# Optimization experiments

Hardware: AMD Instinct MI355X
Metric: run time of the kernel (lower is better)

Reference implementation:

```python
import jax, jax.numpy as jnp
import numpy as np
from jax import lax

B, N, C = 16, 16384, 256
NP, NS = 128, 16        # num_proposal, nsample
R = 0.3                 # ball radius (normalize_xyz divides by R)


def setup_inputs() -> dict:
    key = jax.random.key(0)
    ks = jax.random.split(key, 11)
    f32 = jnp.float32
    return dict(
        vote_xyz=jax.random.uniform(ks[0], (B, N, 3), f32),
        vote_features=jax.random.normal(ks[1], (B, C, N), f32),
        # SA shared-MLP 1x1 conv weights (bias folded into BN), mlp=[259,128,128,128]
        W1=jax.random.normal(ks[2], (128, C + 3), f32) * 0.05,
        W2=jax.random.normal(ks[3], (128, 128), f32) * 0.05,
        W3=jax.random.normal(ks[4], (128, 128), f32) * 0.05,
        sa_bn_scale=jax.random.uniform(ks[5], (3, 128), f32, 0.5, 1.5),
        sa_bn_bias=jax.random.normal(ks[6], (3, 128), f32) * 0.1,
        # trailing mlp_module: two Conv1d(128,128,1)+BN(eval)+ReLU
        Wm=jax.random.normal(ks[7], (2, 128, 128), f32) * 0.05,
        bm=jax.random.normal(ks[8], (2, 128), f32) * 0.01,
        m_bn_scale=jax.random.uniform(ks[9], (2, 128), f32, 0.5, 1.5),
        m_bn_bias=jax.random.normal(ks[10], (2, 128), f32) * 0.1,
    )


def _fps(xyz):
    # farthest point sampling, one cloud: xyz [N,3] -> inds [NP]
    def body(carry, _):
        mind, last = carry
        d = jnp.sum((xyz - xyz[last]) ** 2, axis=-1)
        mind = jnp.minimum(mind, d)
        nxt = jnp.argmax(mind).astype(jnp.int32)
        return (mind, nxt), nxt
    init = (jnp.full((xyz.shape[0],), 1e10, xyz.dtype), jnp.int32(0))
    _, rest = lax.scan(body, init, None, length=NP - 1)
    return jnp.concatenate([jnp.zeros((1,), jnp.int32), rest])


def _ball_query(xyz, centers):
    # xyz [N,3], centers [NP,3] -> idx [NP,NS]; first NS in-ball points in
    # original order, padded with the first in-ball index (pointnet2 semantics)
    d2 = jnp.sum((centers[:, None, :] - xyz[None, :, :]) ** 2, axis=-1)  # [NP,N]
    n = xyz.shape[0]
    cand = jnp.where(d2 < R * R, jnp.arange(n, dtype=jnp.int32), jnp.int32(n))
    firstk = jnp.sort(cand, axis=-1)[:, :NS]                             # [NP,NS]
    first = firstk[:, :1]
    idx = jnp.where(firstk == n, first, firstk)
    return jnp.where(idx == n, 0, idx)


def _forward(vote_xyz, vote_features, W1, W2, W3, sa_bn_scale, sa_bn_bias,
             Wm, bm, m_bn_scale, m_bn_bias):
    fps_inds = jax.vmap(_fps)(vote_xyz)                                   # [B,NP]
    new_xyz = jnp.take_along_axis(vote_xyz, fps_inds[..., None], axis=1)  # [B,NP,3]
    idx = jax.vmap(_ball_query)(vote_xyz, new_xyz)                        # [B,NP,NS]
    grouped_xyz = jax.vmap(lambda p, i: p[i])(vote_xyz, idx)              # [B,NP,NS,3]
    grouped_xyz = (grouped_xyz - new_xyz[:, :, None, :]) / R              # normalize_xyz
    grouped_feat = jax.vmap(lambda f, i: f[:, i])(vote_features, idx)     # [B,C,NP,NS]
    g = jnp.concatenate([grouped_xyz.transpose(0, 3, 1, 2), grouped_feat], axis=1)  # [B,C+3,NP,NS]
    for W, s, b in ((W1, sa_bn_scale[0], sa_bn_bias[0]),
                    (W2, sa_bn_scale[1], sa_bn_bias[1]),
                    (W3, sa_bn_scale[2], sa_bn_bias[2])):
        g = jax.nn.relu(jnp.einsum('bcsn,oc->bosn', g, W)
                        * s[None, :, None, None] + b[None, :, None, None])
    feat = jnp.max(g, axis=-1)                                            # [B,128,NP] max pool
    for k in range(2):
        feat = jax.nn.relu((jnp.einsum('bcs,oc->bos', feat, Wm[k]) + bm[k][None, :, None])
                           * m_bn_scale[k][None, :, None] + m_bn_bias[k][None, :, None])
    return new_xyz, feat, fps_inds


def reference(vote_xyz, vote_features, W1, W2, W3, sa_bn_scale, sa_bn_bias,
              Wm, bm, m_bn_scale, m_bn_bias):
    return _forward(vote_xyz, vote_features, W1, W2, W3, sa_bn_scale, sa_bn_bias,
                    Wm, bm, m_bn_scale, m_bn_bias)
```

## Files before the change

### kernel.cpp

```cpp
#include <hip/hip_runtime.h>
#include <hip/hip_bf16.h>

#define NB  16
#define NN  16384
#define NC  256
#define NPP 128
#define NSS 16

#define FTH 1024
#define FPT 16

__global__ __launch_bounds__(256) void transpose_kernel(
    const float* __restrict__ W1, const float* __restrict__ W2,
    const float* __restrict__ W3, const float* __restrict__ Wm,
    float* __restrict__ W1T, float* __restrict__ W2T,
    float* __restrict__ W3T, float* __restrict__ WmT) {
  int i = blockIdx.x * 256 + threadIdx.x;
  if (i < 128 * 259) { int o = i / 259, c = i - o * 259; W1T[c * 128 + o] = W1[i]; }
  if (i < 128 * 128) {
    int o = i >> 7, c = i & 127;
    W2T[c * 128 + o] = W2[i];
    W3T[c * 128 + o] = W3[i];
    WmT[c * 128 + o] = Wm[i];
    WmT[16384 + c * 128 + o] = Wm[16384 + i];
  }
}

__global__ __attribute__((amdgpu_flat_work_group_size(1024, 1024)))
void fps_kernel(
    const float* __restrict__ xyz,
    float* __restrict__ centers, float* __restrict__ out_xyz,
    float* __restrict__ out_indf) {
  int b = blockIdx.x;
  const float* px = xyz + (size_t)b * (NN * 3);
  int t = threadIdx.x;
  __shared__ float2 sxy[NN];
  __shared__ unsigned long long cand[2][16];
  __shared__ float zcand[2][16];
  __shared__ float4 hist[NPP];
  float Zr[FPT], MD[FPT];
#pragma unroll
  for (int j = 0; j < FPT; ++j) {
    int n = t + j * FTH;
    float x = px[n * 3 + 0];
    float y = px[n * 3 + 1];
    float z = px[n * 3 + 2];
    asm volatile("" : "+v"(z));
    sxy[n] = make_float2(x, y);
    Zr[j] = z;
    MD[j] = 1e10f;
  }
  float cx = px[0], cy = px[1], cz = px[2];
  if (t == 0) hist[0] = make_float4(cx, cy, cz, 0.0f);
  __syncthreads();
  for (int it = 1; it < NPP; ++it) {
    float bv = -1.0f;
    float bz = 0.0f;
    int bj = 0;
#pragma unroll
    for (int j = 0; j < FPT; ++j) {
      float2 v = sxy[t + j * FTH];
      float dx = __fsub_rn(v.x, cx);
      float dy = __fsub_rn(v.y, cy);
      float dz = __fsub_rn(Zr[j], cz);
      float d  = __fadd_rn(__fadd_rn(__fmul_rn(dx, dx), __fmul_rn(dy, dy)),
                           __fmul_rn(dz, dz));
      float m = fminf(MD[j], d);
      MD[j] = m;
      if (m > bv) { bv = m; bj = j; bz = Zr[j]; }
    }
    int bi = t + (bj << 10);
    unsigned long long pk =
        (((unsigned long long)__float_as_uint(bv)) << 32) |
        (unsigned long long)(~(unsigned)bi);
#define STEP_ROR(N)                                                         \
    {                                                                       \
      unsigned lo = (unsigned)pk, hi = (unsigned)(pk >> 32);                \
      lo = (unsigned)__builtin_amdgcn_mov_dpp((int)lo, 0x120 | N, 0xF, 0xF, true); \
      hi = (unsigned)__builtin_amdgcn_mov_dpp((int)hi, 0x120 | N, 0xF, 0xF, true); \
      float oz = __int_as_float(__builtin_amdgcn_mov_dpp(                   \
          __float_as_int(bz), 0x120 | N, 0xF, 0xF, true));                  \
      unsigned long long o = ((unsigned long long)hi << 32) | lo;           \
      if (o > pk) { pk = o; bz = oz; }                                      \
    }
    STEP_ROR(1) STEP_ROR(2) STEP_ROR(4) STEP_ROR(8)
    {
      unsigned lo = (unsigned)pk, hi = (unsigned)(pk >> 32);
      lo = (unsigned)__builtin_amdgcn_ds_swizzle((int)lo, 0x401F);
      hi = (unsigned)__builtin_amdgcn_ds_swizzle((int)hi, 0x401F);
      float oz = __int_as_float(
          __builtin_amdgcn_ds_swizzle(__float_as_int(bz), 0x401F));
      unsigned long long o = ((unsigned long long)hi << 32) | lo;
      if (o > pk) { pk = o; bz = oz; }
    }
    {
      unsigned long long o = __shfl_xor(pk, 32, 64);
      float oz = __shfl_xor(bz, 32, 64);
      if (o > pk) { pk = o; bz = oz; }
    }
    int p = it & 1;
    if ((t & 63) == 0) { cand[p][t >> 6] = pk; zcand[p][t >> 6] = bz; }
    __syncthreads();
    pk = cand[p][t & 15];
    bz = zcand[p][t & 15];
    STEP_ROR(1) STEP_ROR(2) STEP_ROR(4) STEP_ROR(8)
#undef STEP_ROR
    int win = (int)(~(unsigned)(pk & 0xFFFFFFFFull));
    win = __builtin_amdgcn_readfirstlane(win);
    float2 wv = sxy[win];
    cx = wv.x;
    cy = wv.y;
    cz = bz;
    if (t == 0) hist[it] = make_float4(cx, cy, cz, (float)win);
  }
  __syncthreads();
  if (t < NPP) {
    float4 h = hist[t];
    centers[(b * NPP + t) * 3 + 0] = h.x;
    centers[(b * NPP + t) * 3 + 1] = h.y;
    centers[(b * NPP + t) * 3 + 2] = h.z;
    out_xyz[(b * NPP + t) * 3 + 0] = h.x;
    out_xyz[(b * NPP + t) * 3 + 1] = h.y;
    out_xyz[(b * NPP + t) * 3 + 2] = h.z;
    out_indf[b * NPP + t] = h.w;
  }
}

__global__ __launch_bounds__(64) void ballq_kernel(
    const float* __restrict__ xyz, const float* __restrict__ centers,
    int* __restrict__ bidx) {
  int bs = blockIdx.x;
  int b = bs >> 7;
  int lane = threadIdx.x;
  const float* px = xyz + (size_t)b * (NN * 3);
  float cx = centers[bs * 3 + 0];
  float cy = centers[bs * 3 + 1];
  float cz = centers[bs * 3 + 2];
  __shared__ int coll[NSS];
  const float rr = 0.09f;
  int have = 0;
  for (int c0 = 0; c0 < NN; c0 += 64) {
    int n = c0 + lane;
    float dx = __fsub_rn(px[n * 3 + 0], cx);
    float dy = __fsub_rn(px[n * 3 + 1], cy);
    float dz = __fsub_rn(px[n * 3 + 2], cz);
    float d2 = __fadd_rn(__fadd_rn(__fmul_rn(dx, dx), __fmul_rn(dy, dy)),
                         __fmul_rn(dz, dz));
    bool in = d2 < rr;
    unsigned long long m = __ballot(in);
    if (in) {
      int pos = have + __popcll(m & ((1ull << lane) - 1ull));
      if (pos < NSS) coll[pos] = n;
    }
    have += __popcll(m);
    if (have >= NSS) break;
  }
  __syncthreads();
  int first = coll[0];
  if (lane < NSS) bidx[bs * NSS + lane] = (lane < have) ? coll[lane] : first;
}

__device__ __forceinline__ void layer_f(const float (*in)[20], int cin,
                                        const float* __restrict__ WT,
                                        const float* __restrict__ sc,
                                        const float* __restrict__ bi,
                                        int o2, int k0, float4& r0, float4& r1) {
  float a0[4] = {0.f, 0.f, 0.f, 0.f};
  float a1[4] = {0.f, 0.f, 0.f, 0.f};
  for (int c = 0; c < cin; ++c) {
    float2 w = *(const float2*)(WT + c * 128 + o2);
    float4 gv = *(const float4*)(&in[c][k0]);
    a0[0] = fmaf(w.x, gv.x, a0[0]);
    a0[1] = fmaf(w.x, gv.y, a0[1]);
    a0[2] = fmaf(w.x, gv.z, a0[2]);
    a0[3] = fmaf(w.x, gv.w, a0[3]);
    a1[0] = fmaf(w.y, gv.x, a1[0]);
    a1[1] = fmaf(w.y, gv.y, a1[1]);
    a1[2] = fmaf(w.y, gv.z, a1[2]);
    a1[3] = fmaf(w.y, gv.w, a1[3]);
  }
  float s0 = sc[o2], s1 = sc[o2 + 1], b0 = bi[o2], b1 = bi[o2 + 1];
  r0.x = fmaxf(fmaf(a0[0], s0, b0), 0.f);
  r0.y = fmaxf(fmaf(a0[1], s0, b0), 0.f);
  r0.z = fmaxf(fmaf(a0[2], s0, b0), 0.f);
  r0.w = fmaxf(fmaf(a0[3], s0, b0), 0.f);
  r1.x = fmaxf(fmaf(a1[0], s1, b1), 0.f);
  r1.y = fmaxf(fmaf(a1[1], s1, b1), 0.f);
  r1.z = fmaxf(fmaf(a1[2], s1, b1), 0.f);
  r1.w = fmaxf(fmaf(a1[3], s1, b1), 0.f);
}

__global__ __launch_bounds__(256) void mlp_kernel(
    const float* __restrict__ xyz, const float* __restrict__ feats,
    const float* __restrict__ centers, const int* __restrict__ bidx,
    const float* __restrict__ W1T, const float* __restrict__ W2T,
    const float* __restrict__ W3T, const float* __restrict__ sa_sc,
    const float* __restrict__ sa_bi, float* __restrict__ feat0) {
  int bs = blockIdx.x;
  int b = bs >> 7;
  int s = bs & 127;
  int tid = threadIdx.x;
  __shared__ float g[259][20];
  __shared__ float h1[128][20];
  __shared__ float h2[128][20];
  __shared__ int kidx[NSS];
  __shared__ float ctr[3];
  if (tid < NSS) kidx[tid] = bidx[bs * NSS + tid];
  if (tid < 3) ctr[tid] = centers[bs * 3 + tid];
  __syncthreads();
  const float* px = xyz + (size_t)b * (NN * 3);
  if (tid < NSS) {
    int n = kidx[tid];
    g[0][tid] = __fdiv_rn(__fsub_rn(px[n * 3 + 0], ctr[0]), 0.3f);
    g[1][tid] = __fdiv_rn(__fsub_rn(px[n * 3 + 1], ctr[1]), 0.3f);
    g[2][tid] = __fdiv_rn(__fsub_rn(px[n * 3 + 2], ctr[2]), 0.3f);
  }
  {
    const float* row = feats + ((size_t)b * NC + tid) * NN;
#pragma unroll
    for (int k = 0; k < NSS; ++k) g[3 + tid][k] = row[kidx[k]];
  }
  __syncthreads();
  int o2 = (tid & 63) * 2;
  int k0 = (tid >> 6) * 4;
  float4 r0, r1;
  layer_f(g, 259, W1T, sa_sc, sa_bi, o2, k0, r0, r1);
  *(float4*)&h1[o2][k0] = r0;
  *(float4*)&h1[o2 + 1][k0] = r1;
  __syncthreads();
  layer_f(h1, 128, W2T, sa_sc + 128, sa_bi + 128, o2, k0, r0, r1);
  *(float4*)&h2[o2][k0] = r0;
  *(float4*)&h2[o2 + 1][k0] = r1;
  __syncthreads();
  layer_f(h2, 128, W3T, sa_sc + 256, sa_bi + 256, o2, k0, r0, r1);
  float m0 = fmaxf(fmaxf(r0.x, r0.y), fmaxf(r0.z, r0.w));
  float m1 = fmaxf(fmaxf(r1.x, r1.y), fmaxf(r1.z, r1.w));
  int w = tid >> 6;
  h1[o2][w] = m0;
  h1[o2 + 1][w] = m1;
  __syncthreads();
  if (tid < 128) {
    float m = fmaxf(fmaxf(h1[tid][0], h1[tid][1]), fmaxf(h1[tid][2], h1[tid][3]));
    feat0[((size_t)b * 128 + tid) * 128 + s] = m;
  }
}

__global__ __launch_bounds__(256) void head_kernel(
    const float* __restrict__ feat0, const float* __restrict__ WmT,
    const float* __restrict__ bm, const float* __restrict__ msc,
    const float* __restrict__ mbi, float* __restrict__ out_feat) {
  int blk = blockIdx.x;
  int b = blk >> 2;
  int sbase = (blk & 3) * 32;
  int tid = threadIdx.x;
  __shared__ float fa[128][36];
  __shared__ float fb[128][36];
  {
    int sj = tid & 31, c0 = tid >> 5;
    for (int c = c0; c < 128; c += 8)
      fa[c][sj] = feat0[((size_t)b * 128 + c) * 128 + sbase + sj];
  }
  __syncthreads();
  int o2 = (tid & 63) * 2, s0 = (tid >> 6) * 8;
  float a0[8], a1[8];
#pragma unroll
  for (int j = 0; j < 8; ++j) { a0[j] = 0.f; a1[j] = 0.f; }
  for (int c = 0; c < 128; ++c) {
    float2 w = *(const float2*)&WmT[c * 128 + o2];
    float4 f0 = *(const float4*)&fa[c][s0];
    float4 f1 = *(const float4*)&fa[c][s0 + 4];
    a0[0] = fmaf(w.x, f0.x, a0[0]); a0[1] = fmaf(w.x, f0.y, a0[1]);
    a0[2] = fmaf(w.x, f0.z, a0[2]); a0[3] = fmaf(w.x, f0.w, a0[3]);
    a0[4] = fmaf(w.x, f1.x, a0[4]); a0[5] = fmaf(w.x, f1.y, a0[5]);
    a0[6] = fmaf(w.x, f1.z, a0[6]); a0[7] = fmaf(w.x, f1.w, a0[7]);
    a1[0] = fmaf(w.y, f0.x, a1[0]); a1[1] = fmaf(w.y, f0.y, a1[1]);
    a1[2] = fmaf(w.y, f0.z, a1[2]); a1[3] = fmaf(w.y, f0.w, a1[3]);
    a1[4] = fmaf(w.y, f1.x, a1[4]); a1[5] = fmaf(w.y, f1.y, a1[5]);
    a1[6] = fmaf(w.y, f1.z, a1[6]); a1[7] = fmaf(w.y, f1.w, a1[7]);
  }
  {
    float c0 = bm[o2], c1 = bm[o2 + 1];
    float t0 = msc[o2], t1 = msc[o2 + 1];
    float q0 = mbi[o2], q1 = mbi[o2 + 1];
#pragma unroll
    for (int j = 0; j < 8; ++j) {
      fb[o2][s0 + j]     = fmaxf(fmaf(a0[j] + c0, t0, q0), 0.f);
      fb[o2 + 1][s0 + j] = fmaxf(fmaf(a1[j] + c1, t1, q1), 0.f);
    }
  }
  __syncthreads();
#pragma unroll
  for (int j = 0; j < 8; ++j) { a0[j] = 0.f; a1[j] = 0.f; }
  for (int c = 0; c < 128; ++c) {
    float2 w = *(const float2*)&WmT[16384 + c * 128 + o2];
    float4 f0 = *(const float4*)&fb[c][s0];
    float4 f1 = *(const float4*)&fb[c][s0 + 4];
    a0[0] = fmaf(w.x, f0.x, a0[0]); a0[1] = fmaf(w.x, f0.y, a0[1]);
    a0[2] = fmaf(w.x, f0.z, a0[2]); a0[3] = fmaf(w.x, f0.w, a0[3]);
    a0[4] = fmaf(w.x, f1.x, a0[4]); a0[5] = fmaf(w.x, f1.y, a0[5]);
    a0[6] = fmaf(w.x, f1.z, a0[6]); a0[7] = fmaf(w.x, f1.w, a0[7]);
    a1[0] = fmaf(w.y, f0.x, a1[0]); a1[1] = fmaf(w.y, f0.y, a1[1]);
    a1[2] = fmaf(w.y, f0.z, a1[2]); a1[3] = fmaf(w.y, f0.w, a1[3]);
    a1[4] = fmaf(w.y, f1.x, a1[4]); a1[5] = fmaf(w.y, f1.y, a1[5]);
    a1[6] = fmaf(w.y, f1.z, a1[6]); a1[7] = fmaf(w.y, f1.w, a1[7]);
  }
  {
    float c0 = bm[128 + o2], c1 = bm[128 + o2 + 1];
    float t0 = msc[128 + o2], t1 = msc[128 + o2 + 1];
    float q0 = mbi[128 + o2], q1 = mbi[128 + o2 + 1];
    float4 v0a, v0b, v1a, v1b;
    v0a.x = fmaxf(fmaf(a0[0] + c0, t0, q0), 0.f);
    v0a.y = fmaxf(fmaf(a0[1] + c0, t0, q0), 0.f);
    v0a.z = fmaxf(fmaf(a0[2] + c0, t0, q0), 0.f);
    v0a.w = fmaxf(fmaf(a0[3] + c0, t0, q0), 0.f);
    v0b.x = fmaxf(fmaf(a0[4] + c0, t0, q0), 0.f);
    v0b.y = fmaxf(fmaf(a0[5] + c0, t0, q0), 0.f);
    v0b.z = fmaxf(fmaf(a0[6] + c0, t0, q0), 0.f);
    v0b.w = fmaxf(fmaf(a0[7] + c0, t0, q0), 0.f);
    v1a.x = fmaxf(fmaf(a1[0] + c1, t1, q1), 0.f);
    v1a.y = fmaxf(fmaf(a1[1] + c1, t1, q1), 0.f);
    v1a.z = fmaxf(fmaf(a1[2] + c1, t1, q1), 0.f);
    v1a.w = fmaxf(fmaf(a1[3] + c1, t1, q1), 0.f);
    v1b.x = fmaxf(fmaf(a1[4] + c1, t1, q1), 0.f);
    v1b.y = fmaxf(fmaf(a1[5] + c1, t1, q1), 0.f);
    v1b.z = fmaxf(fmaf(a1[6] + c1, t1, q1), 0.f);
    v1b.w = fmaxf(fmaf(a1[7] + c1, t1, q1), 0.f);
    float* p0 = &out_feat[((size_t)b * 128 + o2) * 128 + sbase + s0];
    float* p1 = &out_feat[((size_t)b * 128 + o2 + 1) * 128 + sbase + s0];
    *(float4*)p0 = v0a;
    *(float4*)(p0 + 4) = v0b;
    *(float4*)p1 = v1a;
    *(float4*)(p1 + 4) = v1b;
  }
}

extern "C" void kernel_launch(void* const* d_in, const int* in_sizes, int n_in,
                              void* d_out, int out_size, void* d_ws, size_t ws_size,
                              hipStream_t stream) {
  const float* vote_xyz  = (const float*)d_in[0];
  const float* vote_feat = (const float*)d_in[1];
  const float* W1   = (const float*)d_in[2];
  const float* W2   = (const float*)d_in[3];
  const float* W3   = (const float*)d_in[4];
  const float* sasc = (const float*)d_in[5];
  const float* sabi = (const float*)d_in[6];
  const float* Wm   = (const float*)d_in[7];
  const float* bm   = (const float*)d_in[8];
  const float* msc  = (const float*)d_in[9];
  const float* mbi  = (const float*)d_in[10];

  float* out = (float*)d_out;
  float* out_xyz  = out;
  float* out_feat = out + 6144;
  float* out_indf = out + 6144 + 262144;

  char* ws = (char*)d_ws;
  float* centers = (float*)(ws + 8192);
  int*   bidx    = (int*)(ws + 32768);
  float* W1T     = (float*)(ws + 163840);
  float* W2T     = (float*)(ws + 296448);
  float* W3T     = (float*)(ws + 361984);
  float* WmT     = (float*)(ws + 427520);
  float* feat0   = (float*)(ws + 558592);

  hipLaunchKernelGGL(transpose_kernel, dim3(130), dim3(256), 0, stream,
                     W1, W2, W3, Wm, W1T, W2T, W3T, WmT);
  hipLaunchKernelGGL(fps_kernel, dim3(NB), dim3(FTH), 0, stream,
                     vote_xyz, centers, out_xyz, out_indf);
  hipLaunchKernelGGL(ballq_kernel, dim3(NB * NPP), dim3(64), 0, stream,
                     vote_xyz, centers, bidx);
  hipLaunchKernelGGL(mlp_kernel, dim3(NB * NPP), dim3(256), 0, stream,
                     vote_xyz, vote_feat, centers, bidx, W1T, W2T, W3T,
                     sasc, sabi, feat0);
  hipLaunchKernelGGL(head_kernel, dim3(NB * 4), dim3(256), 0, stream,
                     feat0, WmT, bm, msc, mbi, out_feat);
}
```

Baseline: 430.2 us.

## Keep half of FPS coordinates in registers and widen MLP per-thread tile

The FPS kernel now keeps the x/y coordinates of the first 8 of each thread's 16 points in registers and puts only the other half in shared memory. It drops propagation of the winning z through the reductions and instead reads the winner's coordinates from global memory. The MLP kernel moves to 128 threads, each computing 4 output channels by 4 samples, and reuses the g buffer for h2. The aim is less LDS traffic and fewer shuffles in the serial FPS loop and more arithmetic per weight load in the MLP, at the cost of higher register pressure and a global-load latency on the FPS critical path each iteration.

```diff
diff --git a/kernel.cpp b/kernel.cpp
--- a/kernel.cpp
+++ b/kernel.cpp
@@ -8,7 +8,6 @@
 #define NSS 16
 
 #define FTH 1024
-#define FPT 16
 
 __global__ __launch_bounds__(256) void transpose_kernel(
     const float* __restrict__ W1, const float* __restrict__ W2,
@@ -34,19 +33,23 @@
   int b = blockIdx.x;
   const float* px = xyz + (size_t)b * (NN * 3);
   int t = threadIdx.x;
-  __shared__ float2 sxy[NN];
+  __shared__ float2 sxy[NN / 2];
   __shared__ unsigned long long cand[2][16];
-  __shared__ float zcand[2][16];
   __shared__ float4 hist[NPP];
-  float Zr[FPT], MD[FPT];
-#pragma unroll
-  for (int j = 0; j < FPT; ++j) {
-    int n = t + j * FTH;
+  float Xr[8], Yr[8], Zr[16], MD[16];
+#pragma unroll
+  for (int j = 0; j < 16; ++j) {
+    int n = t + (j << 10);
     float x = px[n * 3 + 0];
     float y = px[n * 3 + 1];
     float z = px[n * 3 + 2];
     asm volatile("" : "+v"(z));
-    sxy[n] = make_float2(x, y);
+    if (j < 8) {
+      asm volatile("" : "+v"(x), "+v"(y));
+      Xr[j] = x; Yr[j] = y;
+    } else {
+      sxy[n - 8192] = make_float2(x, y);
+    }
     Zr[j] = z;
     MD[j] = 1e10f;
   }
@@ -55,11 +58,21 @@
   __syncthreads();
   for (int it = 1; it < NPP; ++it) {
     float bv = -1.0f;
-    float bz = 0.0f;
-    int bj = 0;
-#pragma unroll
-    for (int j = 0; j < FPT; ++j) {
-      float2 v = sxy[t + j * FTH];
+    int bi = 0;
+#pragma unroll
+    for (int j = 0; j < 8; ++j) {
+      float dx = __fsub_rn(Xr[j], cx);
+      float dy = __fsub_rn(Yr[j], cy);
+      float dz = __fsub_rn(Zr[j], cz);
+      float d  = __fadd_rn(__fadd_rn(__fmul_rn(dx, dx), __fmul_rn(dy, dy)),
+                           __fmul_rn(dz, dz));
+      float m = fminf(MD[j], d);
+      MD[j] = m;
+      if (m > bv) { bv = m; bi = t + (j << 10); }
+    }
+#pragma unroll
+    for (int j = 8; j < 16; ++j) {
+      float2 v = sxy[t + ((j - 8) << 10)];
       float dx = __fsub_rn(v.x, cx);
       float dy = __fsub_rn(v.y, cy);
       float dz = __fsub_rn(Zr[j], cz);
@@ -67,9 +80,8 @@
                            __fmul_rn(dz, dz));
       float m = fminf(MD[j], d);
       MD[j] = m;
-      if (m > bv) { bv = m; bj = j; bz = Zr[j]; }
-    }
-    int bi = t + (bj << 10);
+      if (m > bv) { bv = m; bi = t + (j << 10); }
+    }
     unsigned long long pk =
         (((unsigned long long)__float_as_uint(bv)) << 32) |
         (unsigned long long)(~(unsigned)bi);
@@ -78,39 +90,32 @@
       unsigned lo = (unsigned)pk, hi = (unsigned)(pk >> 32);                \
       lo = (unsigned)__builtin_amdgcn_mov_dpp((int)lo, 0x120 | N, 0xF, 0xF, true); \
       hi = (unsigned)__builtin_amdgcn_mov_dpp((int)hi, 0x120 | N, 0xF, 0xF, true); \
-      float oz = __int_as_float(__builtin_amdgcn_mov_dpp(                   \
-          __float_as_int(bz), 0x120 | N, 0xF, 0xF, true));                  \
       unsigned long long o = ((unsigned long long)hi << 32) | lo;           \
-      if (o > pk) { pk = o; bz = oz; }                                      \
+      if (o > pk) pk = o;                                                   \
     }
     STEP_ROR(1) STEP_ROR(2) STEP_ROR(4) STEP_ROR(8)
     {
       unsigned lo = (unsigned)pk, hi = (unsigned)(pk >> 32);
       lo = (unsigned)__builtin_amdgcn_ds_swizzle((int)lo, 0x401F);
       hi = (unsigned)__builtin_amdgcn_ds_swizzle((int)hi, 0x401F);
-      float oz = __int_as_float(
-          __builtin_amdgcn_ds_swizzle(__float_as_int(bz), 0x401F));
       unsigned long long o = ((unsigned long long)hi << 32) | lo;
-      if (o > pk) { pk = o; bz = oz; }
+      if (o > pk) pk = o;
     }
     {
       unsigned long long o = __shfl_xor(pk, 32, 64);
-      float oz = __shfl_xor(bz, 32, 64);
-      if (o > pk) { pk = o; bz = oz; }
+      if (o > pk) pk = o;
     }
     int p = it & 1;
-    if ((t & 63) == 0) { cand[p][t >> 6] = pk; zcand[p][t >> 6] = bz; }
+    if ((t & 63) == 0) cand[p][t >> 6] = pk;
     __syncthreads();
     pk = cand[p][t & 15];
-    bz = zcand[p][t & 15];
     STEP_ROR(1) STEP_ROR(2) STEP_ROR(4) STEP_ROR(8)
 #undef STEP_ROR
     int win = (int)(~(unsigned)(pk & 0xFFFFFFFFull));
     win = __builtin_amdgcn_readfirstlane(win);
-    float2 wv = sxy[win];
-    cx = wv.x;
-    cy = wv.y;
-    cz = bz;
+    cx = px[win * 3 + 0];
+    cy = px[win * 3 + 1];
+    cz = px[win * 3 + 2];
     if (t == 0) hist[it] = make_float4(cx, cy, cz, (float)win);
   }
   __syncthreads();
@@ -160,37 +165,42 @@
   if (lane < NSS) bidx[bs * NSS + lane] = (lane < have) ? coll[lane] : first;
 }
 
-__device__ __forceinline__ void layer_f(const float (*in)[20], int cin,
-                                        const float* __restrict__ WT,
-                                        const float* __restrict__ sc,
-                                        const float* __restrict__ bi,
-                                        int o2, int k0, float4& r0, float4& r1) {
-  float a0[4] = {0.f, 0.f, 0.f, 0.f};
-  float a1[4] = {0.f, 0.f, 0.f, 0.f};
+__device__ __forceinline__ float4 bnrelu4(float4 a, float s, float b) {
+  float4 r;
+  r.x = fmaxf(fmaf(a.x, s, b), 0.f);
+  r.y = fmaxf(fmaf(a.y, s, b), 0.f);
+  r.z = fmaxf(fmaf(a.z, s, b), 0.f);
+  r.w = fmaxf(fmaf(a.w, s, b), 0.f);
+  return r;
+}
+
+__device__ __forceinline__ void layer4(const float (*in)[20], int cin,
+                                       const float* __restrict__ WT,
+                                       const float* __restrict__ sc,
+                                       const float* __restrict__ bi,
+                                       int o4, int k0,
+                                       float4& r0, float4& r1,
+                                       float4& r2, float4& r3) {
+  float4 a0 = {0.f, 0.f, 0.f, 0.f}, a1 = a0, a2 = a0, a3 = a0;
   for (int c = 0; c < cin; ++c) {
-    float2 w = *(const float2*)(WT + c * 128 + o2);
+    float4 w  = *(const float4*)(WT + c * 128 + o4);
     float4 gv = *(const float4*)(&in[c][k0]);
-    a0[0] = fmaf(w.x, gv.x, a0[0]);
-    a0[1] = fmaf(w.x, gv.y, a0[1]);
-    a0[2] = fmaf(w.x, gv.z, a0[2]);
-    a0[3] = fmaf(w.x, gv.w, a0[3]);
-    a1[0] = fmaf(w.y, gv.x, a1[0]);
-    a1[1] = fmaf(w.y, gv.y, a1[1]);
-    a1[2] = fmaf(w.y, gv.z, a1[2]);
-    a1[3] = fmaf(w.y, gv.w, a1[3]);
-  }
-  float s0 = sc[o2], s1 = sc[o2 + 1], b0 = bi[o2], b1 = bi[o2 + 1];
-  r0.x = fmaxf(fmaf(a0[0], s0, b0), 0.f);
-  r0.y = fmaxf(fmaf(a0[1], s0, b0), 0.f);
-  r0.z = fmaxf(fmaf(a0[2], s0, b0), 0.f);
-  r0.w = fmaxf(fmaf(a0[3], s0, b0), 0.f);
-  r1.x = fmaxf(fmaf(a1[0], s1, b1), 0.f);
-  r1.y = fmaxf(fmaf(a1[1], s1, b1), 0.f);
-  r1.z = fmaxf(fmaf(a1[2], s1, b1), 0.f);
-  r1.w = fmaxf(fmaf(a1[3], s1, b1), 0.f);
-}
-
-__global__ __launch_bounds__(256) void mlp_kernel(
+    a0.x = fmaf(w.x, gv.x, a0.x); a0.y = fmaf(w.x, gv.y, a0.y);
+    a0.z = fmaf(w.x, gv.z, a0.z); a0.w = fmaf(w.x, gv.w, a0.w);
+    a1.x = fmaf(w.y, gv.x, a1.x); a1.y = fmaf(w.y, gv.y, a1.y);
+    a1.z = fmaf(w.y, gv.z, a1.z); a1.w = fmaf(w.y, gv.w, a1.w);
+    a2.x = fmaf(w.z, gv.x, a2.x); a2.y = fmaf(w.z, gv.y, a2.y);
+    a2.z = fmaf(w.z, gv.z, a2.z); a2.w = fmaf(w.z, gv.w, a2.w);
+    a3.x = fmaf(w.w, gv.x, a3.x); a3.y = fmaf(w.w, gv.y, a3.y);
+    a3.z = fmaf(w.w, gv.z, a3.z); a3.w = fmaf(w.w, gv.w, a3.w);
+  }
+  r0 = bnrelu4(a0, sc[o4 + 0], bi[o4 + 0]);
+  r1 = bnrelu4(a1, sc[o4 + 1], bi[o4 + 1]);
+  r2 = bnrelu4(a2, sc[o4 + 2], bi[o4 + 2]);
+  r3 = bnrelu4(a3, sc[o4 + 3], bi[o4 + 3]);
+}
+
+__global__ __launch_bounds__(128) void mlp_kernel(
     const float* __restrict__ xyz, const float* __restrict__ feats,
     const float* __restrict__ centers, const int* __restrict__ bidx,
     const float* __restrict__ W1T, const float* __restrict__ W2T,
@@ -200,9 +210,9 @@
   int b = bs >> 7;
   int s = bs & 127;
   int tid = threadIdx.x;
-  __shared__ float g[259][20];
-  __shared__ float h1[128][20];
-  __shared__ float h2[128][20];
+  __shared__ __align__(16) float g[259][20];
+  __shared__ __align__(16) float h1[128][20];
+  float (*h2)[20] = (float (*)[20]) & g[0][0];
   __shared__ int kidx[NSS];
   __shared__ float ctr[3];
   if (tid < NSS) kidx[tid] = bidx[bs * NSS + tid];
@@ -215,29 +225,40 @@
     g[1][tid] = __fdiv_rn(__fsub_rn(px[n * 3 + 1], ctr[1]), 0.3f);
     g[2][tid] = __fdiv_rn(__fsub_rn(px[n * 3 + 2], ctr[2]), 0.3f);
   }
-  {
-    const float* row = feats + ((size_t)b * NC + tid) * NN;
-#pragma unroll
-    for (int k = 0; k < NSS; ++k) g[3 + tid][k] = row[kidx[k]];
-  }
-  __syncthreads();
-  int o2 = (tid & 63) * 2;
-  int k0 = (tid >> 6) * 4;
-  float4 r0, r1;
-  layer_f(g, 259, W1T, sa_sc, sa_bi, o2, k0, r0, r1);
-  *(float4*)&h1[o2][k0] = r0;
-  *(float4*)&h1[o2 + 1][k0] = r1;
-  __syncthreads();
-  layer_f(h1, 128, W2T, sa_sc + 128, sa_bi + 128, o2, k0, r0, r1);
-  *(float4*)&h2[o2][k0] = r0;
-  *(float4*)&h2[o2 + 1][k0] = r1;
-  __syncthreads();
-  layer_f(h2, 128, W3T, sa_sc + 256, sa_bi + 256, o2, k0, r0, r1);
+#pragma unroll
+  for (int cc = 0; cc < 2; ++cc) {
+    int c = tid + cc * 128;
+    const float* row = feats + ((size_t)b * NC + c) * NN;
+#pragma unroll
+    for (int k = 0; k < NSS; ++k) g[3 + c][k] = row[kidx[k]];
+  }
+  __syncthreads();
+  int o4 = (tid & 31) * 4;
+  int k0 = (tid >> 5) * 4;
+  float4 r0, r1, r2, r3;
+  layer4(g, 259, W1T, sa_sc, sa_bi, o4, k0, r0, r1, r2, r3);
+  *(float4*)&h1[o4 + 0][k0] = r0;
+  *(float4*)&h1[o4 + 1][k0] = r1;
+  *(float4*)&h1[o4 + 2][k0] = r2;
+  *(float4*)&h1[o4 + 3][k0] = r3;
+  __syncthreads();
+  layer4(h1, 128, W2T, sa_sc + 128, sa_bi + 128, o4, k0, r0, r1, r2, r3);
+  __syncthreads();
+  *(float4*)&h2[o4 + 0][k0] = r0;
+  *(float4*)&h2[o4 + 1][k0] = r1;
+  *(float4*)&h2[o4 + 2][k0] = r2;
+  *(float4*)&h2[o4 + 3][k0] = r3;
+  __syncthreads();
+  layer4(h2, 128, W3T, sa_sc + 256, sa_bi + 256, o4, k0, r0, r1, r2, r3);
   float m0 = fmaxf(fmaxf(r0.x, r0.y), fmaxf(r0.z, r0.w));
   float m1 = fmaxf(fmaxf(r1.x, r1.y), fmaxf(r1.z, r1.w));
-  int w = tid >> 6;
-  h1[o2][w] = m0;
-  h1[o2 + 1][w] = m1;
+  float m2 = fmaxf(fmaxf(r2.x, r2.y), fmaxf(r2.z, r2.w));
+  float m3 = fmaxf(fmaxf(r3.x, r3.y), fmaxf(r3.z, r3.w));
+  int kg = tid >> 5;
+  h1[o4 + 0][kg] = m0;
+  h1[o4 + 1][kg] = m1;
+  h1[o4 + 2][kg] = m2;
+  h1[o4 + 3][kg] = m3;
   __syncthreads();
   if (tid < 128) {
     float m = fmaxf(fmaxf(h1[tid][0], h1[tid][1]), fmaxf(h1[tid][2], h1[tid][3]));
@@ -369,7 +390,7 @@
                      vote_xyz, centers, out_xyz, out_indf);
   hipLaunchKernelGGL(ballq_kernel, dim3(NB * NPP), dim3(64), 0, stream,
                      vote_xyz, centers, bidx);
-  hipLaunchKernelGGL(mlp_kernel, dim3(NB * NPP), dim3(256), 0, stream,
+  hipLaunchKernelGGL(mlp_kernel, dim3(NB * NPP), dim3(128), 0, stream,
                      vote_xyz, vote_feat, centers, bidx, W1T, W2T, W3T,
                      sasc, sabi, feat0);
   hipLaunchKernelGGL(head_kernel, dim3(NB * 4), dim3(256), 0, stream,
```

Result: faster. 362.1 us (-15.8%).
